# Performance work log

Measured on AMD Instinct MI355X. Metric: run time of the kernel, lower is better.

The kernel has to match this reference:

```python
import jax, jax.numpy as jnp
import numpy as np

EPS = 1e-5
SLOPE = 0.1


def _leaky(v):
    return jnp.where(v >= 0, v, SLOPE * v)


def _bn(v, gamma, beta):
    # v: (C, Q, k); training-mode batch norm over (Q, k) with biased variance
    m = v.mean(axis=(1, 2), keepdims=True)
    var = v.var(axis=(1, 2), keepdims=True)
    return (v - m) * jax.lax.rsqrt(var + EPS) * gamma[:, None, None] + beta[:, None, None]


def setup_inputs() -> dict:
    key = jax.random.key(0)
    ks = jax.random.split(key, 6)
    Q, S, K, F, O = 16384, 16384, 32, 64, 64
    q_points = jax.random.normal(ks[0], (Q, 3), dtype=jnp.float32)
    s_points = jax.random.normal(ks[1], (S, 3), dtype=jnp.float32)
    neighb_inds = jax.random.randint(ks[2], (Q, K), 0, S + 1)  # S is the padded zero row
    feat = jax.random.normal(ks[3], (S, F), dtype=jnp.float32)
    conv0_w = jax.random.normal(ks[4], (O, F), dtype=jnp.float32) * 0.1
    conv1_w = jax.random.normal(ks[5], (O * 3, O), dtype=jnp.float32) * 0.1
    return {
        "q_points": q_points,
        "s_points": s_points,
        "feat": feat,
        "neighb_inds": neighb_inds,
        "conv0_w": conv0_w,
        "gamma0": jnp.ones((O,), jnp.float32),
        "beta0": jnp.zeros((O,), jnp.float32),
        "conv1_w": conv1_w,
        "gamma1": jnp.ones((O,), jnp.float32),
        "beta1": jnp.zeros((O,), jnp.float32),
    }


def reference(q_points, s_points, feat, neighb_inds, conv0_w, gamma0, beta0, conv1_w, gamma1, beta1):
    Q, K = neighb_inds.shape
    n_supports = s_points.shape[0]
    out_c = conv1_w.shape[1]
    in_c = conv1_w.shape[0] // out_c  # = 3 for feat_mode='xyz'

    # pad with a zero row (index n_supports is the 'out of range' shadow point)
    s_pad = jnp.concatenate([s_points, jnp.zeros((1, s_points.shape[1]), s_points.dtype)], 0)
    f_pad = jnp.concatenate([feat, jnp.zeros((1, feat.shape[1]), feat.dtype)], 0)

    # relative xyz feature; zero out shadow neighbors
    x = s_pad[neighb_inds] - q_points[:, None, :]          # (Q, K, 3)
    mask = (neighb_inds == n_supports)[..., None]
    x = jnp.where(mask, jnp.zeros((), x.dtype), x)

    y = f_pad[neighb_inds]                                  # (Q, K, F)

    # kernel generation: conv0 (1x1) -> BN -> LeakyReLU -> conv1 (1x1)
    h = jnp.einsum('of,qkf->oqk', conv0_w, y)               # (O, Q, K)
    h = _leaky(_bn(h, gamma0, beta0))
    ker = jnp.einsum('co,oqk->qkc', conv1_w, h)             # (Q, K, O*in_c)
    ker = ker.reshape(Q, K, out_c, in_c)                    # (Q, K, O, 3)

    # per-edge matmul against relative xyz, then BN -> LeakyReLU -> max over k
    z = jnp.einsum('qkoi,qki->oqk', ker, x)                 # (O, Q, K)
    z = _leaky(_bn(z, gamma1, beta1))
    z = z.max(axis=2)                                       # (O, Q)
    return z.T                                              # (Q, O)
```

## Files before the change

### kernel.cpp

```cpp
#include <hip/hip_runtime.h>
#include <hip/hip_bf16.h>

typedef __attribute__((ext_vector_type(8))) short bf16x8;
typedef __attribute__((ext_vector_type(4))) short bf16x4;
typedef __attribute__((ext_vector_type(4))) float f32x4;

#define LEAKY(v) ((v) >= 0.f ? (v) : 0.1f * (v))

constexpr int Q = 16384, S = 16384, KNN = 32, F = 64, O = 64;
constexpr int NEDGE = Q * KNN;
constexpr int QB = 8;
constexpr int EB = 256;
constexpr int GD = Q / QB;
constexpr int GH = 128;
constexpr int FP = 72;
constexpr float EPSV = 1e-5f;

constexpr size_t CNT_OFF  = 0;
constexpr size_t CTR_OFF  = 65536;
constexpr size_t P0_OFF   = 65600;
constexpr size_t ST0_OFF  = P0_OFF + (size_t)GH * 128 * 4;
constexpr size_t ZMIN_OFF = ST0_OFF + 512;
constexpr size_t P1_OFF   = ZMIN_OFF + (size_t)Q * O * 4;
constexpr size_t ST1_OFF  = P1_OFF + (size_t)GD * 128 * 4;
constexpr size_t W0F_OFF  = ST1_OFF + 512;
constexpr size_t W1F_OFF  = W0F_OFF + 8192;

__device__ __forceinline__ short f2bf(float f) {
  __hip_bfloat16 h = __float2bfloat16(f);
  short r; __builtin_memcpy(&r, &h, 2); return r;
}

__global__ void k_prep_hist(const float* __restrict__ w0g, const float* __restrict__ w1g,
                            short* __restrict__ w0f, short* __restrict__ w1f,
                            const int* __restrict__ inds, int* __restrict__ cnt) {
  if (blockIdx.x < 8) {
    const int t = blockIdx.x * 256 + threadIdx.x;
    const int fa = t >> 6, ln = t & 63;
    const int l4 = ln >> 4, l15 = ln & 15;
    if (fa < 8) {
      const int mt = fa >> 1, kk = fa & 1;
      const int o = 16 * mt + l15, f = 32 * kk + 8 * l4;
      const float* src = w0g + o * 64 + f;
      bf16x8 pk;
#pragma unroll
      for (int j = 0; j < 8; ++j) pk[j] = f2bf(src[j]);
      *(bf16x8*)&w0f[t * 8] = pk;
    } else {
      const int fb = fa - 8;
      const int nt = fb >> 1, kk = fb & 1;
      const int i = nt >> 2, b = nt & 3;
      const int o = 16 * b + l15, op = 32 * kk + 8 * l4;
      const float* src = w1g + (o * 3 + i) * 64 + op;
      bf16x8 pk;
#pragma unroll
      for (int j = 0; j < 8; ++j) pk[j] = f2bf(src[j]);
      *(bf16x8*)&w1f[(fb * 64 + ln) * 8] = pk;
    }
  } else {
    const int i = (blockIdx.x - 8) * 256 + threadIdx.x;
    const int4 v = ((const int4*)inds)[i];
    if (v.x < S) atomicAdd(&cnt[v.x], 1);
    if (v.y < S) atomicAdd(&cnt[v.y], 1);
    if (v.z < S) atomicAdd(&cnt[v.z], 1);
    if (v.w < S) atomicAdd(&cnt[v.w], 1);
  }
}

__global__ void k_hsq(const float* __restrict__ feat, const int* __restrict__ cnt,
                      const short* __restrict__ w0f, float* __restrict__ p0,
                      int* __restrict__ ctr, const float* __restrict__ g0,
                      const float* __restrict__ b0, float* __restrict__ st0) {
  __shared__ float sred[4][2][64];
  __shared__ int isLast;
  const int t = threadIdx.x, blk = blockIdx.x;
  const int wv = t >> 6, ln = t & 63, l4 = ln >> 4, l15 = ln & 15;

  const bf16x8* w0v = (const bf16x8*)w0f;
  bf16x8 w0a[8];
#pragma unroll
  for (int fa = 0; fa < 8; ++fa) w0a[fa] = w0v[fa * 64 + ln];

  float hs[4][4], hq[4][4];
#pragma unroll
  for (int mt = 0; mt < 4; ++mt)
#pragma unroll
    for (int r = 0; r < 4; ++r) { hs[mt][r] = 0.f; hq[mt][r] = 0.f; }

#pragma unroll
  for (int tile = 0; tile < 2; ++tile) {
    const int s0 = blk * 128 + (wv * 2 + tile) * 16;
    const float wc = (float)cnt[s0 + l15];
    const float4* fr = (const float4*)(feat + (size_t)(s0 + l15) * 64);
    float4 a = fr[2 * l4], b = fr[2 * l4 + 1];
    float4 c = fr[8 + 2 * l4], d = fr[9 + 2 * l4];
    bf16x8 y0, y1;
    y0[0] = f2bf(a.x); y0[1] = f2bf(a.y); y0[2] = f2bf(a.z); y0[3] = f2bf(a.w);
    y0[4] = f2bf(b.x); y0[5] = f2bf(b.y); y0[6] = f2bf(b.z); y0[7] = f2bf(b.w);
    y1[0] = f2bf(c.x); y1[1] = f2bf(c.y); y1[2] = f2bf(c.z); y1[3] = f2bf(c.w);
    y1[4] = f2bf(d.x); y1[5] = f2bf(d.y); y1[6] = f2bf(d.z); y1[7] = f2bf(d.w);
#pragma unroll
    for (int mt = 0; mt < 4; ++mt) {
      f32x4 acc = {0.f, 0.f, 0.f, 0.f};
      acc = __builtin_amdgcn_mfma_f32_16x16x32_bf16(w0a[2 * mt], y0, acc, 0, 0, 0);
      acc = __builtin_amdgcn_mfma_f32_16x16x32_bf16(w0a[2 * mt + 1], y1, acc, 0, 0, 0);
#pragma unroll
      for (int r = 0; r < 4; ++r) {
        float h = acc[r];
        hs[mt][r] += wc * h;
        hq[mt][r] += wc * h * h;
      }
    }
  }
#pragma unroll
  for (int mt = 0; mt < 4; ++mt)
#pragma unroll
    for (int r = 0; r < 4; ++r) {
      float s = hs[mt][r], q = hq[mt][r];
#pragma unroll
      for (int d = 1; d < 16; d <<= 1) { s += __shfl_xor(s, d); q += __shfl_xor(q, d); }
      hs[mt][r] = s; hq[mt][r] = q;
    }
  if (l15 == 0) {
#pragma unroll
    for (int mt = 0; mt < 4; ++mt)
#pragma unroll
      for (int r = 0; r < 4; ++r) {
        const int o = 16 * mt + 4 * l4 + r;
        sred[wv][0][o] = hs[mt][r];
        sred[wv][1][o] = hq[mt][r];
      }
  }
  __syncthreads();
  if (t < 128) {
    const int qq = t >> 6, o = t & 63;
    p0[(size_t)blk * 128 + t] =
        sred[0][qq][o] + sred[1][qq][o] + sred[2][qq][o] + sred[3][qq][o];
  }
  __syncthreads();
  __threadfence();
  if (t == 0) isLast = (atomicAdd(&ctr[0], 1) == GH - 1);
  __syncthreads();
  if (isLast) {
    __threadfence();
    if (t < O) {
      float s = 0.f, q = 0.f;
      for (int b = 0; b < GH; ++b) {
        s += p0[(size_t)b * 128 + t];
        q += p0[(size_t)b * 128 + 64 + t];
      }
      const float invN = 1.f / (float)NEDGE;
      float mean = s * invN;
      float var = q * invN - mean * mean;
      float sc = g0[t] * rsqrtf(var + EPSV);
      st0[t] = sc;
      st0[O + t] = b0[t] - mean * sc;
    }
  }
}

__launch_bounds__(256, 3)
__global__ void k_main(const float* __restrict__ qpts, const float* __restrict__ spts,
                       const float* __restrict__ feat, const int* __restrict__ inds,
                       const short* __restrict__ w0f, const short* __restrict__ w1f,
                       const float* __restrict__ st0,
                       float* __restrict__ zmax, float* __restrict__ zmin,
                       float* __restrict__ p1) {
  __shared__ __align__(16) short hbuf[EB * FP];
  __shared__ __align__(16) float xs[3 * EB];

  const int t = threadIdx.x, blk = blockIdx.x;
  const int wv = t >> 6, ln = t & 63, l4 = ln >> 4, l15 = ln & 15;
  const int ebase = blk * EB;

  {
    const int e = t;
    const int idx = inds[ebase + e];
    const int q = blk * QB + (e >> 5);
    float x0 = 0.f, x1 = 0.f, x2 = 0.f;
    if (idx < S) {
      x0 = spts[idx * 3 + 0] - qpts[q * 3 + 0];
      x1 = spts[idx * 3 + 1] - qpts[q * 3 + 1];
      x2 = spts[idx * 3 + 2] - qpts[q * 3 + 2];
    }
    xs[0 * EB + e] = x0; xs[1 * EB + e] = x1; xs[2 * EB + e] = x2;
  }

  float scr[4][4], shr[4][4];
#pragma unroll
  for (int mt = 0; mt < 4; ++mt)
#pragma unroll
    for (int r = 0; r < 4; ++r) {
      int o = 16 * mt + 4 * l4 + r;
      scr[mt][r] = st0[o]; shr[mt][r] = st0[O + o];
    }

  const bf16x8* w0v = (const bf16x8*)w0f;
  bf16x8 w0a[8];
#pragma unroll
  for (int fa = 0; fa < 8; ++fa) w0a[fa] = w0v[fa * 64 + ln];

#pragma unroll
  for (int nt = 0; nt < 4; ++nt) {
    const int erow = wv * 64 + nt * 16 + l15;
    const int idx = inds[ebase + erow];
    bf16x8 y0, y1;
    if (idx < S) {
      const float* fr = feat + (size_t)idx * F + 8 * l4;
      f32x4 a = *(const f32x4*)(fr);
      f32x4 b = *(const f32x4*)(fr + 4);
      f32x4 c = *(const f32x4*)(fr + 32);
      f32x4 d = *(const f32x4*)(fr + 36);
      y0[0] = f2bf(a[0]); y0[1] = f2bf(a[1]); y0[2] = f2bf(a[2]); y0[3] = f2bf(a[3]);
      y0[4] = f2bf(b[0]); y0[5] = f2bf(b[1]); y0[6] = f2bf(b[2]); y0[7] = f2bf(b[3]);
      y1[0] = f2bf(c[0]); y1[1] = f2bf(c[1]); y1[2] = f2bf(c[2]); y1[3] = f2bf(c[3]);
      y1[4] = f2bf(d[0]); y1[5] = f2bf(d[1]); y1[6] = f2bf(d[2]); y1[7] = f2bf(d[3]);
    } else {
#pragma unroll
      for (int j = 0; j < 8; ++j) { y0[j] = 0; y1[j] = 0; }
    }
#pragma unroll
    for (int mt = 0; mt < 4; ++mt) {
      f32x4 acc = {0.f, 0.f, 0.f, 0.f};
      acc = __builtin_amdgcn_mfma_f32_16x16x32_bf16(w0a[2 * mt], y0, acc, 0, 0, 0);
      acc = __builtin_amdgcn_mfma_f32_16x16x32_bf16(w0a[2 * mt + 1], y1, acc, 0, 0, 0);
      bf16x4 hv;
#pragma unroll
      for (int r = 0; r < 4; ++r) {
        float v = acc[r] * scr[mt][r] + shr[mt][r];
        v = LEAKY(v);
        hv[r] = f2bf(v);
      }
      *(bf16x4*)&hbuf[erow * FP + 16 * mt + 4 * l4] = hv;
    }
  }

  bf16x8 hA[4][2];
#pragma unroll
  for (int mt = 0; mt < 4; ++mt) {
    const int erow = wv * 64 + mt * 16 + l15;
    hA[mt][0] = *(const bf16x8*)&hbuf[erow * FP + 8 * l4];
    hA[mt][1] = *(const bf16x8*)&hbuf[erow * FP + 32 + 8 * l4];
  }

  const bf16x8* w1v = (const bf16x8*)w1f;
  float zmx[2][4], zmn[2][4], zs[4], zq[4];
#pragma unroll
  for (int j = 0; j < 4; ++j) {
    zs[j] = 0.f; zq[j] = 0.f;
    zmx[0][j] = -3.4e38f; zmx[1][j] = -3.4e38f;
    zmn[0][j] = 3.4e38f;  zmn[1][j] = 3.4e38f;
  }

#pragma unroll
  for (int b = 0; b < 4; ++b) {
    bf16x8 w1b[6];
#pragma unroll
    for (int i = 0; i < 3; ++i)
#pragma unroll
      for (int kk = 0; kk < 2; ++kk)
        w1b[i * 2 + kk] = w1v[(((i * 4 + b) * 2) + kk) * 64 + ln];
#pragma unroll
    for (int mt = 0; mt < 4; ++mt) {
      const int ex = wv * 64 + mt * 16 + 4 * l4;
      f32x4 z4 = {0.f, 0.f, 0.f, 0.f};
#pragma unroll
      for (int i = 0; i < 3; ++i) {
        f32x4 acc = {0.f, 0.f, 0.f, 0.f};
        acc = __builtin_amdgcn_mfma_f32_16x16x32_bf16(hA[mt][0], w1b[2 * i], acc, 0, 0, 0);
        acc = __builtin_amdgcn_mfma_f32_16x16x32_bf16(hA[mt][1], w1b[2 * i + 1], acc, 0, 0, 0);
        const f32x4 xv = *(const f32x4*)&xs[i * EB + ex];
#pragma unroll
        for (int r = 0; r < 4; ++r) z4[r] += acc[r] * xv[r];
      }
      const int qh = mt >> 1;
#pragma unroll
      for (int r = 0; r < 4; ++r) {
        float v = z4[r];
        zmx[qh][b] = fmaxf(zmx[qh][b], v);
        zmn[qh][b] = fminf(zmn[qh][b], v);
        zs[b] += v; zq[b] += v * v;
      }
    }
  }

#pragma unroll
  for (int qh = 0; qh < 2; ++qh)
#pragma unroll
    for (int b = 0; b < 4; ++b) {
      float m = zmx[qh][b];
      m = fmaxf(m, __shfl_xor(m, 16)); m = fmaxf(m, __shfl_xor(m, 32));
      zmx[qh][b] = m;
      float n = zmn[qh][b];
      n = fminf(n, __shfl_xor(n, 16)); n = fminf(n, __shfl_xor(n, 32));
      zmn[qh][b] = n;
    }
#pragma unroll
  for (int b = 0; b < 4; ++b) {
    float s = zs[b];  s += __shfl_xor(s, 16);  s += __shfl_xor(s, 32);  zs[b] = s;
    float sq = zq[b]; sq += __shfl_xor(sq, 16); sq += __shfl_xor(sq, 32); zq[b] = sq;
  }

  if (l4 == 0) {
#pragma unroll
    for (int qh = 0; qh < 2; ++qh) {
      const int q = blk * QB + wv * 2 + qh;
#pragma unroll
      for (int b = 0; b < 4; ++b) {
        zmax[(size_t)q * O + 16 * b + l15] = zmx[qh][b];
        zmin[(size_t)q * O + 16 * b + l15] = zmn[qh][b];
      }
    }
  }

  __syncthreads();
  if (l4 == 0) {
#pragma unroll
    for (int b = 0; b < 4; ++b) {
      xs[wv * 128 + 16 * b + l15] = zs[b];
      xs[wv * 128 + 64 + 16 * b + l15] = zq[b];
    }
  }
  __syncthreads();
  if (t < 128)
    p1[(size_t)blk * 128 + t] = xs[t] + xs[128 + t] + xs[256 + t] + xs[384 + t];
}

__global__ void k_red1(const float* __restrict__ p1, const float* __restrict__ g1,
                       const float* __restrict__ b1, float* __restrict__ st1) {
  __shared__ float rs[256], rq[256];
  const int o = blockIdx.x, t = threadIdx.x;
  float s = 0.f, q = 0.f;
  for (int r = t; r < GD; r += 256) {
    s += p1[(size_t)r * 128 + o];
    q += p1[(size_t)r * 128 + 64 + o];
  }
  rs[t] = s; rq[t] = q;
  __syncthreads();
  for (int off = 128; off > 0; off >>= 1) {
    if (t < off) { rs[t] += rs[t + off]; rq[t] += rq[t + off]; }
    __syncthreads();
  }
  if (t == 0) {
    const float invN = 1.f / (float)NEDGE;
    float mean = rs[0] * invN;
    float var = rq[0] * invN - mean * mean;
    float sc = g1[o] * rsqrtf(var + EPSV);
    st1[o] = sc;
    st1[O + o] = b1[o] - mean * sc;
  }
}

__global__ void k_final(const float* __restrict__ st1, const float* __restrict__ zmin,
                        float* __restrict__ out) {
  int i = blockIdx.x * blockDim.x + threadIdx.x;
  if (i < Q * O) {
    int o = i & 63;
    float sc = st1[o], sh = st1[O + o];
    float base = (sc >= 0.f) ? out[i] : zmin[i];
    float v = base * sc + sh;
    out[i] = LEAKY(v);
  }
}

extern "C" void kernel_launch(void* const* d_in, const int* in_sizes, int n_in,
                              void* d_out, int out_size, void* d_ws, size_t ws_size,
                              hipStream_t stream) {
  const float* qpts = (const float*)d_in[0];
  const float* spts = (const float*)d_in[1];
  const float* feat = (const float*)d_in[2];
  const int*   inds = (const int*)d_in[3];
  const float* w0   = (const float*)d_in[4];
  const float* g0   = (const float*)d_in[5];
  const float* b0   = (const float*)d_in[6];
  const float* w1   = (const float*)d_in[7];
  const float* g1   = (const float*)d_in[8];
  const float* b1   = (const float*)d_in[9];
  float* out = (float*)d_out;

  char* ws = (char*)d_ws;
  int*   cnt  = (int*)(ws + CNT_OFF);
  int*   ctr  = (int*)(ws + CTR_OFF);
  float* p0   = (float*)(ws + P0_OFF);
  float* st0  = (float*)(ws + ST0_OFF);
  float* zmin = (float*)(ws + ZMIN_OFF);
  float* p1   = (float*)(ws + P1_OFF);
  float* st1  = (float*)(ws + ST1_OFF);
  short* w0f  = (short*)(ws + W0F_OFF);
  short* w1f  = (short*)(ws + W1F_OFF);

  hipMemsetAsync(ws, 0, CTR_OFF + 64, stream);
  k_prep_hist<<<520, 256, 0, stream>>>(w0, w1, w0f, w1f, inds, cnt);
  k_hsq<<<GH, 256, 0, stream>>>(feat, cnt, w0f, p0, ctr, g0, b0, st0);
  k_main<<<GD, 256, 0, stream>>>(qpts, spts, feat, inds, w0f, w1f, st0, out, zmin, p1);
  k_red1<<<64, 256, 0, stream>>>(p1, g1, b1, st1);
  k_final<<<(Q * O) / 256, 256, 0, stream>>>(st1, zmin, out);
}
```

Measured before the change: 94.65 us.

## Pre-convert features to bf16, privatize histogram in LDS, transpose partials, vectorize final

Features are converted to bf16 once in the prep kernel, so k_main gathers half the bytes per neighbour and does no per-edge conversion. All feature loads are also issued up front. The index histogram is built in a per-block shared-memory histogram before flushing to global, which cuts global atomic contention. The BN1 partials are stored transposed so k_red1 reads them coalesced, and k_final is vectorized to four elements per thread. The cost is an extra 2 MB bf16 feature buffer and a 64 KB LDS histogram per block.

```diff
diff --git a/kernel.cpp b/kernel.cpp
--- a/kernel.cpp
+++ b/kernel.cpp
@@ -4,27 +4,26 @@
 typedef __attribute__((ext_vector_type(8))) short bf16x8;
 typedef __attribute__((ext_vector_type(4))) short bf16x4;
 typedef __attribute__((ext_vector_type(4))) float f32x4;
-
-#define LEAKY(v) ((v) >= 0.f ? (v) : 0.1f * (v))
 
 constexpr int Q = 16384, S = 16384, KNN = 32, F = 64, O = 64;
 constexpr int NEDGE = Q * KNN;
 constexpr int QB = 8;
 constexpr int EB = 256;
 constexpr int GD = Q / QB;
-constexpr int GH = 128;
+constexpr int GH = 256;
 constexpr int FP = 72;
 constexpr float EPSV = 1e-5f;
 
-constexpr size_t CNT_OFF  = 0;
-constexpr size_t CTR_OFF  = 65536;
-constexpr size_t P0_OFF   = 65600;
-constexpr size_t ST0_OFF  = P0_OFF + (size_t)GH * 128 * 4;
-constexpr size_t ZMIN_OFF = ST0_OFF + 512;
-constexpr size_t P1_OFF   = ZMIN_OFF + (size_t)Q * O * 4;
-constexpr size_t ST1_OFF  = P1_OFF + (size_t)GD * 128 * 4;
-constexpr size_t W0F_OFF  = ST1_OFF + 512;
-constexpr size_t W1F_OFF  = W0F_OFF + 8192;
+constexpr size_t CNT_OFF   = 0;
+constexpr size_t CTR_OFF   = 65536;
+constexpr size_t P0_OFF    = 65600;
+constexpr size_t ST0_OFF   = P0_OFF + (size_t)GH * 128 * 4;
+constexpr size_t ZMIN_OFF  = ST0_OFF + 512;
+constexpr size_t P1T_OFF   = ZMIN_OFF + (size_t)Q * O * 4;
+constexpr size_t ST1_OFF   = P1T_OFF + (size_t)128 * GD * 4;
+constexpr size_t W0F_OFF   = ST1_OFF + 512;
+constexpr size_t W1F_OFF   = W0F_OFF + 8192;
+constexpr size_t FEATB_OFF = W1F_OFF + 24576;
 
 __device__ __forceinline__ short f2bf(float f) {
   __hip_bfloat16 h = __float2bfloat16(f);
@@ -33,9 +32,12 @@
 
 __global__ void k_prep_hist(const float* __restrict__ w0g, const float* __restrict__ w1g,
                             short* __restrict__ w0f, short* __restrict__ w1f,
+                            const float* __restrict__ feat, short* __restrict__ featb,
                             const int* __restrict__ inds, int* __restrict__ cnt) {
-  if (blockIdx.x < 8) {
-    const int t = blockIdx.x * 256 + threadIdx.x;
+  __shared__ int lh[S];
+  const int bx = blockIdx.x, tt = threadIdx.x;
+  if (bx < 8) {
+    const int t = bx * 256 + tt;
     const int fa = t >> 6, ln = t & 63;
     const int l4 = ln >> 4, l15 = ln & 15;
     if (fa < 8) {
@@ -57,17 +59,40 @@
       for (int j = 0; j < 8; ++j) pk[j] = f2bf(src[j]);
       *(bf16x8*)&w1f[(fb * 64 + ln) * 8] = pk;
     }
+  } else if (bx < 72) {
+    const int base = (bx - 8) * 16384;
+#pragma unroll
+    for (int j = 0; j < 8; ++j) {
+      const int i = base + j * 2048 + tt * 8;
+      f32x4 a = *(const f32x4*)(feat + i);
+      f32x4 b = *(const f32x4*)(feat + i + 4);
+      bf16x8 pk;
+      pk[0] = f2bf(a[0]); pk[1] = f2bf(a[1]); pk[2] = f2bf(a[2]); pk[3] = f2bf(a[3]);
+      pk[4] = f2bf(b[0]); pk[5] = f2bf(b[1]); pk[6] = f2bf(b[2]); pk[7] = f2bf(b[3]);
+      *(bf16x8*)(featb + i) = pk;
+    }
   } else {
-    const int i = (blockIdx.x - 8) * 256 + threadIdx.x;
-    const int4 v = ((const int4*)inds)[i];
-    if (v.x < S) atomicAdd(&cnt[v.x], 1);
-    if (v.y < S) atomicAdd(&cnt[v.y], 1);
-    if (v.z < S) atomicAdd(&cnt[v.z], 1);
-    if (v.w < S) atomicAdd(&cnt[v.w], 1);
-  }
-}
-
-__global__ void k_hsq(const float* __restrict__ feat, const int* __restrict__ cnt,
+    for (int c = tt; c < S; c += 256) lh[c] = 0;
+    __syncthreads();
+    const int4* ip = (const int4*)inds;
+    const int base = (bx - 72) * 2048;
+#pragma unroll
+    for (int j = 0; j < 8; ++j) {
+      const int4 v = ip[base + j * 256 + tt];
+      if (v.x < S) atomicAdd(&lh[v.x], 1);
+      if (v.y < S) atomicAdd(&lh[v.y], 1);
+      if (v.z < S) atomicAdd(&lh[v.z], 1);
+      if (v.w < S) atomicAdd(&lh[v.w], 1);
+    }
+    __syncthreads();
+    for (int c = tt; c < S; c += 256) {
+      const int v = lh[c];
+      if (v) atomicAdd(&cnt[c], v);
+    }
+  }
+}
+
+__global__ void k_hsq(const short* __restrict__ featb, const int* __restrict__ cnt,
                       const short* __restrict__ w0f, float* __restrict__ p0,
                       int* __restrict__ ctr, const float* __restrict__ g0,
                       const float* __restrict__ b0, float* __restrict__ st0) {
@@ -81,35 +106,23 @@
 #pragma unroll
   for (int fa = 0; fa < 8; ++fa) w0a[fa] = w0v[fa * 64 + ln];
 
+  const int s0 = blk * 64 + wv * 16;
+  const float wc = (float)cnt[s0 + l15];
+  const short* fb = featb + (size_t)(s0 + l15) * F + 8 * l4;
+  const bf16x8 y0 = *(const bf16x8*)(fb);
+  const bf16x8 y1 = *(const bf16x8*)(fb + 32);
+
   float hs[4][4], hq[4][4];
 #pragma unroll
-  for (int mt = 0; mt < 4; ++mt)
-#pragma unroll
-    for (int r = 0; r < 4; ++r) { hs[mt][r] = 0.f; hq[mt][r] = 0.f; }
-
-#pragma unroll
-  for (int tile = 0; tile < 2; ++tile) {
-    const int s0 = blk * 128 + (wv * 2 + tile) * 16;
-    const float wc = (float)cnt[s0 + l15];
-    const float4* fr = (const float4*)(feat + (size_t)(s0 + l15) * 64);
-    float4 a = fr[2 * l4], b = fr[2 * l4 + 1];
-    float4 c = fr[8 + 2 * l4], d = fr[9 + 2 * l4];
-    bf16x8 y0, y1;
-    y0[0] = f2bf(a.x); y0[1] = f2bf(a.y); y0[2] = f2bf(a.z); y0[3] = f2bf(a.w);
-    y0[4] = f2bf(b.x); y0[5] = f2bf(b.y); y0[6] = f2bf(b.z); y0[7] = f2bf(b.w);
-    y1[0] = f2bf(c.x); y1[1] = f2bf(c.y); y1[2] = f2bf(c.z); y1[3] = f2bf(c.w);
-    y1[4] = f2bf(d.x); y1[5] = f2bf(d.y); y1[6] = f2bf(d.z); y1[7] = f2bf(d.w);
-#pragma unroll
-    for (int mt = 0; mt < 4; ++mt) {
-      f32x4 acc = {0.f, 0.f, 0.f, 0.f};
-      acc = __builtin_amdgcn_mfma_f32_16x16x32_bf16(w0a[2 * mt], y0, acc, 0, 0, 0);
-      acc = __builtin_amdgcn_mfma_f32_16x16x32_bf16(w0a[2 * mt + 1], y1, acc, 0, 0, 0);
-#pragma unroll
-      for (int r = 0; r < 4; ++r) {
-        float h = acc[r];
-        hs[mt][r] += wc * h;
-        hq[mt][r] += wc * h * h;
-      }
+  for (int mt = 0; mt < 4; ++mt) {
+    f32x4 acc = {0.f, 0.f, 0.f, 0.f};
+    acc = __builtin_amdgcn_mfma_f32_16x16x32_bf16(w0a[2 * mt], y0, acc, 0, 0, 0);
+    acc = __builtin_amdgcn_mfma_f32_16x16x32_bf16(w0a[2 * mt + 1], y1, acc, 0, 0, 0);
+#pragma unroll
+    for (int r = 0; r < 4; ++r) {
+      const float h = acc[r];
+      hs[mt][r] = wc * h;
+      hq[mt][r] = wc * h * h;
     }
   }
 #pragma unroll
@@ -150,9 +163,9 @@
         q += p0[(size_t)b * 128 + 64 + t];
       }
       const float invN = 1.f / (float)NEDGE;
-      float mean = s * invN;
-      float var = q * invN - mean * mean;
-      float sc = g0[t] * rsqrtf(var + EPSV);
+      const float mean = s * invN;
+      const float var = q * invN - mean * mean;
+      const float sc = g0[t] * rsqrtf(var + EPSV);
       st0[t] = sc;
       st0[O + t] = b0[t] - mean * sc;
     }
@@ -161,11 +174,11 @@
 
 __launch_bounds__(256, 3)
 __global__ void k_main(const float* __restrict__ qpts, const float* __restrict__ spts,
-                       const float* __restrict__ feat, const int* __restrict__ inds,
+                       const short* __restrict__ featb, const int* __restrict__ inds,
                        const short* __restrict__ w0f, const short* __restrict__ w1f,
                        const float* __restrict__ st0,
                        float* __restrict__ zmax, float* __restrict__ zmin,
-                       float* __restrict__ p1) {
+                       float* __restrict__ p1t) {
   __shared__ __align__(16) short hbuf[EB * FP];
   __shared__ __align__(16) float xs[3 * EB];
 
@@ -186,49 +199,50 @@
     xs[0 * EB + e] = x0; xs[1 * EB + e] = x1; xs[2 * EB + e] = x2;
   }
 
-  float scr[4][4], shr[4][4];
-#pragma unroll
-  for (int mt = 0; mt < 4; ++mt)
-#pragma unroll
-    for (int r = 0; r < 4; ++r) {
-      int o = 16 * mt + 4 * l4 + r;
-      scr[mt][r] = st0[o]; shr[mt][r] = st0[O + o];
-    }
-
   const bf16x8* w0v = (const bf16x8*)w0f;
   bf16x8 w0a[8];
 #pragma unroll
   for (int fa = 0; fa < 8; ++fa) w0a[fa] = w0v[fa * 64 + ln];
 
+  int idxr[4];
+#pragma unroll
+  for (int nt = 0; nt < 4; ++nt) idxr[nt] = inds[ebase + wv * 64 + nt * 16 + l15];
+
+  bf16x8 yv[4][2];
+#pragma unroll
+  for (int nt = 0; nt < 4; ++nt) {
+    if (idxr[nt] < S) {
+      const short* fb = featb + (size_t)idxr[nt] * F + 8 * l4;
+      yv[nt][0] = *(const bf16x8*)(fb);
+      yv[nt][1] = *(const bf16x8*)(fb + 32);
+    } else {
+#pragma unroll
+      for (int j = 0; j < 8; ++j) { yv[nt][0][j] = 0; yv[nt][1][j] = 0; }
+    }
+  }
+
+  float scr[4][4], shr[4][4];
+#pragma unroll
+  for (int mt = 0; mt < 4; ++mt)
+#pragma unroll
+    for (int r = 0; r < 4; ++r) {
+      const int o = 16 * mt + 4 * l4 + r;
+      scr[mt][r] = st0[o]; shr[mt][r] = st0[O + o];
+    }
+
 #pragma unroll
   for (int nt = 0; nt < 4; ++nt) {
     const int erow = wv * 64 + nt * 16 + l15;
-    const int idx = inds[ebase + erow];
-    bf16x8 y0, y1;
-    if (idx < S) {
-      const float* fr = feat + (size_t)idx * F + 8 * l4;
-      f32x4 a = *(const f32x4*)(fr);
-      f32x4 b = *(const f32x4*)(fr + 4);
-      f32x4 c = *(const f32x4*)(fr + 32);
-      f32x4 d = *(const f32x4*)(fr + 36);
-      y0[0] = f2bf(a[0]); y0[1] = f2bf(a[1]); y0[2] = f2bf(a[2]); y0[3] = f2bf(a[3]);
-      y0[4] = f2bf(b[0]); y0[5] = f2bf(b[1]); y0[6] = f2bf(b[2]); y0[7] = f2bf(b[3]);
-      y1[0] = f2bf(c[0]); y1[1] = f2bf(c[1]); y1[2] = f2bf(c[2]); y1[3] = f2bf(c[3]);
-      y1[4] = f2bf(d[0]); y1[5] = f2bf(d[1]); y1[6] = f2bf(d[2]); y1[7] = f2bf(d[3]);
-    } else {
-#pragma unroll
-      for (int j = 0; j < 8; ++j) { y0[j] = 0; y1[j] = 0; }
-    }
 #pragma unroll
     for (int mt = 0; mt < 4; ++mt) {
       f32x4 acc = {0.f, 0.f, 0.f, 0.f};
-      acc = __builtin_amdgcn_mfma_f32_16x16x32_bf16(w0a[2 * mt], y0, acc, 0, 0, 0);
-      acc = __builtin_amdgcn_mfma_f32_16x16x32_bf16(w0a[2 * mt + 1], y1, acc, 0, 0, 0);
+      acc = __builtin_amdgcn_mfma_f32_16x16x32_bf16(w0a[2 * mt], yv[nt][0], acc, 0, 0, 0);
+      acc = __builtin_amdgcn_mfma_f32_16x16x32_bf16(w0a[2 * mt + 1], yv[nt][1], acc, 0, 0, 0);
       bf16x4 hv;
 #pragma unroll
       for (int r = 0; r < 4; ++r) {
         float v = acc[r] * scr[mt][r] + shr[mt][r];
-        v = LEAKY(v);
+        v = fmaxf(v, 0.1f * v);
         hv[r] = f2bf(v);
       }
       *(bf16x4*)&hbuf[erow * FP + 16 * mt + 4 * l4] = hv;
@@ -276,7 +290,7 @@
       const int qh = mt >> 1;
 #pragma unroll
       for (int r = 0; r < 4; ++r) {
-        float v = z4[r];
+        const float v = z4[r];
         zmx[qh][b] = fmaxf(zmx[qh][b], v);
         zmn[qh][b] = fminf(zmn[qh][b], v);
         zs[b] += v; zq[b] += v * v;
@@ -323,17 +337,20 @@
   }
   __syncthreads();
   if (t < 128)
-    p1[(size_t)blk * 128 + t] = xs[t] + xs[128 + t] + xs[256 + t] + xs[384 + t];
-}
-
-__global__ void k_red1(const float* __restrict__ p1, const float* __restrict__ g1,
+    p1t[(size_t)t * GD + blk] = xs[t] + xs[128 + t] + xs[256 + t] + xs[384 + t];
+}
+
+__global__ void k_red1(const float* __restrict__ p1t, const float* __restrict__ g1,
                        const float* __restrict__ b1, float* __restrict__ st1) {
   __shared__ float rs[256], rq[256];
   const int o = blockIdx.x, t = threadIdx.x;
+  const float* ps = p1t + (size_t)o * GD;
+  const float* pq = p1t + (size_t)(64 + o) * GD;
   float s = 0.f, q = 0.f;
-  for (int r = t; r < GD; r += 256) {
-    s += p1[(size_t)r * 128 + o];
-    q += p1[(size_t)r * 128 + 64 + o];
+#pragma unroll
+  for (int j = 0; j < GD / 256; ++j) {
+    s += ps[j * 256 + t];
+    q += pq[j * 256 + t];
   }
   rs[t] = s; rq[t] = q;
   __syncthreads();
@@ -343,9 +360,9 @@
   }
   if (t == 0) {
     const float invN = 1.f / (float)NEDGE;
-    float mean = rs[0] * invN;
-    float var = rq[0] * invN - mean * mean;
-    float sc = g1[o] * rsqrtf(var + EPSV);
+    const float mean = rs[0] * invN;
+    const float var = rq[0] * invN - mean * mean;
+    const float sc = g1[o] * rsqrtf(var + EPSV);
     st1[o] = sc;
     st1[O + o] = b1[o] - mean * sc;
   }
@@ -353,14 +370,20 @@
 
 __global__ void k_final(const float* __restrict__ st1, const float* __restrict__ zmin,
                         float* __restrict__ out) {
-  int i = blockIdx.x * blockDim.x + threadIdx.x;
-  if (i < Q * O) {
-    int o = i & 63;
-    float sc = st1[o], sh = st1[O + o];
-    float base = (sc >= 0.f) ? out[i] : zmin[i];
-    float v = base * sc + sh;
-    out[i] = LEAKY(v);
-  }
+  const int i4 = blockIdx.x * blockDim.x + threadIdx.x;
+  const int o0 = (i4 * 4) & 63;
+  const f32x4 mx = *(const f32x4*)(out + (size_t)i4 * 4);
+  const f32x4 mn = *(const f32x4*)(zmin + (size_t)i4 * 4);
+  const f32x4 sc = *(const f32x4*)(st1 + o0);
+  const f32x4 sh = *(const f32x4*)(st1 + O + o0);
+  f32x4 r;
+#pragma unroll
+  for (int j = 0; j < 4; ++j) {
+    const float base = (sc[j] >= 0.f) ? mx[j] : mn[j];
+    const float v = base * sc[j] + sh[j];
+    r[j] = fmaxf(v, 0.1f * v);
+  }
+  *(f32x4*)(out + (size_t)i4 * 4) = r;
 }
 
 extern "C" void kernel_launch(void* const* d_in, const int* in_sizes, int n_in,
@@ -379,20 +402,21 @@
   float* out = (float*)d_out;
 
   char* ws = (char*)d_ws;
-  int*   cnt  = (int*)(ws + CNT_OFF);
-  int*   ctr  = (int*)(ws + CTR_OFF);
-  float* p0   = (float*)(ws + P0_OFF);
-  float* st0  = (float*)(ws + ST0_OFF);
-  float* zmin = (float*)(ws + ZMIN_OFF);
-  float* p1   = (float*)(ws + P1_OFF);
-  float* st1  = (float*)(ws + ST1_OFF);
-  short* w0f  = (short*)(ws + W0F_OFF);
-  short* w1f  = (short*)(ws + W1F_OFF);
+  int*   cnt   = (int*)(ws + CNT_OFF);
+  int*   ctr   = (int*)(ws + CTR_OFF);
+  float* p0    = (float*)(ws + P0_OFF);
+  float* st0   = (float*)(ws + ST0_OFF);
+  float* zmin  = (float*)(ws + ZMIN_OFF);
+  float* p1t   = (float*)(ws + P1T_OFF);
+  float* st1   = (float*)(ws + ST1_OFF);
+  short* w0f   = (short*)(ws + W0F_OFF);
+  short* w1f   = (short*)(ws + W1F_OFF);
+  short* featb = (short*)(ws + FEATB_OFF);
 
   hipMemsetAsync(ws, 0, CTR_OFF + 64, stream);
-  k_prep_hist<<<520, 256, 0, stream>>>(w0, w1, w0f, w1f, inds, cnt);
-  k_hsq<<<GH, 256, 0, stream>>>(feat, cnt, w0f, p0, ctr, g0, b0, st0);
-  k_main<<<GD, 256, 0, stream>>>(qpts, spts, feat, inds, w0f, w1f, st0, out, zmin, p1);
-  k_red1<<<64, 256, 0, stream>>>(p1, g1, b1, st1);
-  k_final<<<(Q * O) / 256, 256, 0, stream>>>(st1, zmin, out);
-}
+  k_prep_hist<<<136, 256, 0, stream>>>(w0, w1, w0f, w1f, feat, featb, inds, cnt);
+  k_hsq<<<GH, 256, 0, stream>>>(featb, cnt, w0f, p0, ctr, g0, b0, st0);
+  k_main<<<GD, 256, 0, stream>>>(qpts, spts, featb, inds, w0f, w1f, st0, out, zmin, p1t);
+  k_red1<<<64, 256, 0, stream>>>(p1t, g1, b1, st1);
+  k_final<<<(Q * O) / 1024, 256, 0, stream>>>(st1, zmin, out);
+}
```

Measured after the change: 86.67 us. -8.4%, faster.
